# Kernel optimization log

Measured on AMD Instinct MI355X. Metric: run time of the kernel, lower is better.

The kernel has to match this reference:

```python
import jax, jax.numpy as jnp
import numpy as np

D_MODEL = 1024
NUM_HEADS = 16
D_K = D_MODEL // NUM_HEADS
NEG_INF = -1000000000.0


def setup_inputs() -> dict:
    key = jax.random.key(0)
    ks = jax.random.split(key, 12)
    B, S = 4, 2048
    scale = 1.0 / np.sqrt(D_MODEL)
    inp = {
        "query": jax.random.normal(ks[0], (B, S, D_MODEL), dtype=jnp.float32),
        "key": jax.random.normal(ks[1], (B, S, D_MODEL), dtype=jnp.float32),
        "value": jax.random.normal(ks[2], (B, S, D_MODEL), dtype=jnp.float32),
        # causal mask: True = keep (matches mask == False -> -1e9 fill)
        "mask": jnp.tril(jnp.ones((S, S), dtype=bool)),
        # torch nn.Linear: y = x @ W.T + b, W shape [out, in]
        "Wq": jax.random.normal(ks[3], (D_MODEL, D_MODEL), dtype=jnp.float32) * scale,
        "bq": jnp.zeros((D_MODEL,), dtype=jnp.float32),
        "Wk": jax.random.normal(ks[4], (D_MODEL, D_MODEL), dtype=jnp.float32) * scale,
        "bk": jnp.zeros((D_MODEL,), dtype=jnp.float32),
        "Wv": jax.random.normal(ks[5], (D_MODEL, D_MODEL), dtype=jnp.float32) * scale,
        "bv": jnp.zeros((D_MODEL,), dtype=jnp.float32),
        "Wo": jax.random.normal(ks[6], (D_MODEL, D_MODEL), dtype=jnp.float32) * scale,
        "bo": jnp.zeros((D_MODEL,), dtype=jnp.float32),
    }
    return inp


def _split_heads(x):
    # [B, S, D] -> [B, H, S, d_k]
    B, S, _ = x.shape
    return x.reshape(B, S, NUM_HEADS, D_K).transpose(0, 2, 1, 3)


def reference(query, key, value, mask, Wq, bq, Wk, bk, Wv, bv, Wo, bo):
    B, S, _ = query.shape
    q = _split_heads(query @ Wq.T + bq)
    k = _split_heads(key @ Wk.T + bk)
    v = _split_heads(value @ Wv.T + bv)
    # scores: [B, H, Sq, Sk]
    scores = jnp.einsum("bhqd,bhkd->bhqk", q, k) / jnp.sqrt(jnp.float32(D_K))
    scores = jnp.where(mask[None, None, :, :], scores, NEG_INF)
    p_attn = jax.nn.softmax(scores, axis=-1)
    x = jnp.einsum("bhqk,bhkd->bhqd", p_attn, v)
    x = x.transpose(0, 2, 1, 3).reshape(B, S, D_MODEL)
    return x @ Wo.T + bo
```

## Files before the change

### kernel.cpp

```cpp
#include <hip/hip_runtime.h>
#include <cstdint>
#include <cstddef>


typedef __attribute__((ext_vector_type(8))) short bf16x8;
typedef __attribute__((ext_vector_type(4))) float f32x4;
typedef __attribute__((ext_vector_type(16))) float f32x16;

__device__ __forceinline__ unsigned short f2bf(float f) {
  union { float f; unsigned u; } x; x.f = f;
  unsigned r = x.u + 0x7FFFu + ((x.u >> 16) & 1u);
  return (unsigned short)(r >> 16);
}

__device__ __forceinline__ unsigned cvtpk_bf16(float lo, float hi) {
  unsigned r;
  asm("v_cvt_pk_bf16_f32 %0, %1, %2" : "=v"(r) : "v"(lo), "v"(hi));
  return r;
}

__device__ __forceinline__ f32x16 mfma32(bf16x8 a, bf16x8 b, f32x16 c) {
  return __builtin_amdgcn_mfma_f32_32x32x16_bf16(a, b, c, 0, 0, 0);
}

__global__ __launch_bounds__(256)
void cast_w(const float* __restrict__ wq, const float* __restrict__ wk,
            const float* __restrict__ wv, const float* __restrict__ wo,
            unsigned short* __restrict__ wqb, unsigned short* __restrict__ wkb,
            unsigned short* __restrict__ wvb, unsigned short* __restrict__ wob) {
  constexpr int W4 = 1024 * 1024 / 4;
  const int i = blockIdx.x * 256 + threadIdx.x;
  const int r = i / W4;
  const int off = i - r * W4;
  const float* src = (r == 0) ? wq : (r == 1) ? wk : (r == 2) ? wv : wo;
  unsigned short* dst = (r == 0) ? wqb : (r == 1) ? wkb : (r == 2) ? wvb : wob;
  const float4 f = ((const float4*)src)[off];
  ushort4 o;
  o.x = f2bf(f.x); o.y = f2bf(f.y); o.z = f2bf(f.z); o.w = f2bf(f.w);
  ((ushort4*)dst)[off] = o;
}

__global__ __launch_bounds__(256)
void gemm_qkv(const float* __restrict__ Aq, const float* __restrict__ Ak,
              const float* __restrict__ Av,
              const unsigned short* __restrict__ Wq, const unsigned short* __restrict__ Wk,
              const unsigned short* __restrict__ Wv,
              const float* __restrict__ bq, const float* __restrict__ bk,
              const float* __restrict__ bv,
              unsigned short* __restrict__ Qp, unsigned short* __restrict__ Kp,
              unsigned short* __restrict__ Vt,
              int M, int N, int K) {
  constexpr int LDR = 72;
  __shared__ unsigned short As[128 * LDR];
  __shared__ unsigned short Bs[128 * LDR];
  const int which = blockIdx.x >> 9;
  const int bid = blockIdx.x & 511;
  const float* Af = (which == 0) ? Aq : (which == 1) ? Ak : Av;
  const unsigned short* Bw = (which == 0) ? Wq : (which == 1) ? Wk : Wv;
  const float* bias = (which == 0) ? bq : (which == 1) ? bk : bv;

  const int tid = threadIdx.x;
  const int lane = tid & 63;
  const int w = tid >> 6;
  const int wm = (w >> 1) * 64;
  const int wn = (w & 1) * 64;
  const int xcd = bid & 7, jj = bid >> 3;
  const int m0 = (xcd * 8 + (jj >> 3)) * 128;
  const int n0 = (jj & 7) * 128;
  const int l15 = lane & 15, l4 = lane >> 4;

  f32x4 acc[4][4] = {};

  for (int k0 = 0; k0 < K; k0 += 64) {
    float4 av[4][2];
    bf16x8 bst[4];
#pragma unroll
    for (int q = 0; q < 4; ++q) {
      const int c = q * 256 + tid;
      const int row = c >> 3, kc = (c & 7) * 8;
      const float4* ap = (const float4*)(Af + (size_t)(m0 + row) * K + k0 + kc);
      av[q][0] = ap[0];
      av[q][1] = ap[1];
      bst[q] = *(const bf16x8*)(Bw + (size_t)(n0 + row) * K + k0 + kc);
    }
    __syncthreads();
#pragma unroll
    for (int q = 0; q < 4; ++q) {
      const int c = q * 256 + tid;
      const int row = c >> 3, kc = (c & 7) * 8;
      union { bf16x8 v; unsigned u[4]; } p;
      p.u[0] = cvtpk_bf16(av[q][0].x, av[q][0].y);
      p.u[1] = cvtpk_bf16(av[q][0].z, av[q][0].w);
      p.u[2] = cvtpk_bf16(av[q][1].x, av[q][1].y);
      p.u[3] = cvtpk_bf16(av[q][1].z, av[q][1].w);
      *(bf16x8*)&As[row * LDR + kc] = p.v;
      *(bf16x8*)&Bs[row * LDR + kc] = bst[q];
    }
    __syncthreads();

#pragma unroll
    for (int kk = 0; kk < 2; ++kk) {
      bf16x8 af[4], bfr[4];
#pragma unroll
      for (int m = 0; m < 4; ++m)
        af[m] = *(const bf16x8*)&As[(wm + m * 16 + l15) * LDR + kk * 32 + l4 * 8];
#pragma unroll
      for (int n = 0; n < 4; ++n)
        bfr[n] = *(const bf16x8*)&Bs[(wn + n * 16 + l15) * LDR + kk * 32 + l4 * 8];
#pragma unroll
      for (int m = 0; m < 4; ++m)
#pragma unroll
        for (int n = 0; n < 4; ++n)
          acc[m][n] = __builtin_amdgcn_mfma_f32_16x16x32_bf16(af[m], bfr[n], acc[m][n], 0, 0, 0);
    }
  }

  const int crow = l4 * 4;
#pragma unroll
  for (int m = 0; m < 4; ++m) {
#pragma unroll
    for (int n = 0; n < 4; ++n) {
      const int col = n0 + wn + n * 16 + l15;
      const float bv_ = bias[col];
      if (which == 2) {
        constexpr int SS = 2048;
        const int rowb = m0 + wm + m * 16 + crow;
        const int b_ = rowb >> 11, s_ = rowb & (SS - 1);
        const int vrow = ((b_ << 4) + (col >> 6)) * 64 + (col & 63);
        uint2 pk;
        pk.x = cvtpk_bf16(acc[m][n][0] + bv_, acc[m][n][1] + bv_);
        pk.y = cvtpk_bf16(acc[m][n][2] + bv_, acc[m][n][3] + bv_);
        *(uint2*)&Vt[(size_t)vrow * SS + s_] = pk;
      } else {
        unsigned short* Cb = (which == 0) ? Qp : Kp;
        const float sc = (which == 0) ? 0.125f * 1.44269504f : 1.0f;
#pragma unroll
        for (int j = 0; j < 4; ++j) {
          const int row = m0 + wm + m * 16 + crow + j;
          Cb[(size_t)row * N + col] = f2bf((acc[m][n][j] + bv_) * sc);
        }
      }
    }
  }
}

__global__ __launch_bounds__(256)
void gemm_out(const unsigned short* __restrict__ Ab,
              const unsigned short* __restrict__ Bw,
              const float* __restrict__ bias,
              float* __restrict__ Cf,
              int M, int N, int K) {
  constexpr int LDR = 72;
  __shared__ unsigned short As[128 * LDR];
  __shared__ unsigned short Bs[128 * LDR];
  const int tid = threadIdx.x;
  const int lane = tid & 63;
  const int w = tid >> 6;
  const int wm = (w >> 1) * 64;
  const int wn = (w & 1) * 64;
  const int bid = blockIdx.x;
  const int xcd = bid & 7, jj = bid >> 3;
  const int m0 = (xcd * 8 + (jj >> 3)) * 128;
  const int n0 = (jj & 7) * 128;
  const int l15 = lane & 15, l4 = lane >> 4;

  f32x4 acc[4][4] = {};

  for (int k0 = 0; k0 < K; k0 += 64) {
    bf16x8 ast[4], bst[4];
#pragma unroll
    for (int q = 0; q < 4; ++q) {
      const int c = q * 256 + tid;
      const int row = c >> 3, kc = (c & 7) * 8;
      ast[q] = *(const bf16x8*)(Ab + (size_t)(m0 + row) * K + k0 + kc);
      bst[q] = *(const bf16x8*)(Bw + (size_t)(n0 + row) * K + k0 + kc);
    }
    __syncthreads();
#pragma unroll
    for (int q = 0; q < 4; ++q) {
      const int c = q * 256 + tid;
      const int row = c >> 3, kc = (c & 7) * 8;
      *(bf16x8*)&As[row * LDR + kc] = ast[q];
      *(bf16x8*)&Bs[row * LDR + kc] = bst[q];
    }
    __syncthreads();

#pragma unroll
    for (int kk = 0; kk < 2; ++kk) {
      bf16x8 af[4], bfr[4];
#pragma unroll
      for (int m = 0; m < 4; ++m)
        af[m] = *(const bf16x8*)&As[(wm + m * 16 + l15) * LDR + kk * 32 + l4 * 8];
#pragma unroll
      for (int n = 0; n < 4; ++n)
        bfr[n] = *(const bf16x8*)&Bs[(wn + n * 16 + l15) * LDR + kk * 32 + l4 * 8];
#pragma unroll
      for (int m = 0; m < 4; ++m)
#pragma unroll
        for (int n = 0; n < 4; ++n)
          acc[m][n] = __builtin_amdgcn_mfma_f32_16x16x32_bf16(af[m], bfr[n], acc[m][n], 0, 0, 0);
    }
  }

  const int crow = l4 * 4;
#pragma unroll
  for (int m = 0; m < 4; ++m) {
#pragma unroll
    for (int n = 0; n < 4; ++n) {
      const int col = n0 + wn + n * 16 + l15;
      const float bv_ = bias[col];
#pragma unroll
      for (int j = 0; j < 4; ++j) {
        const int row = m0 + wm + m * 16 + crow + j;
        Cf[(size_t)row * N + col] = acc[m][n][j] + bv_;
      }
    }
  }
}

__global__ __launch_bounds__(256)
void attn_fwd32b(const unsigned short* __restrict__ Qp,
                 const unsigned short* __restrict__ Kp,
                 const unsigned short* __restrict__ Vt,
                 unsigned short* __restrict__ Xo) {
  constexpr int S = 2048, Dm = 1024;
  const int bh = blockIdx.x & 63;
  const int g  = 15 - (int)(blockIdx.x >> 6);
  const int b = bh >> 4, h = bh & 15;
  const int w = threadIdx.x >> 6;
  const int lane = threadIdx.x & 63;
  const int l31 = lane & 31, hi = lane >> 5;
  const int qb = 4 * g + w;
  const int qrow = qb * 32 + l31;
  const int ntw = qb + 1;
  const int NT = 4 * g + 4;

  const unsigned short* qptr = Qp + (size_t)(b * S + qrow) * Dm + h * 64 + hi * 8;
  bf16x8 qf[4];
#pragma unroll
  for (int c = 0; c < 4; ++c) qf[c] = *(const bf16x8*)(qptr + c * 16);

  const unsigned short* kbase = Kp + (size_t)(b * S) * Dm + h * 64 + hi * 8;
  const unsigned short* vr0 = Vt + (size_t)(bh * 64 + l31) * S + hi * 8;
  const unsigned short* vr1 = vr0 + (size_t)32 * S;

  f32x16 ot0 = {}, ot1 = {};
  float m = -1e30f, l = 0.f;

  auto loadK = [&](bf16x8 (&kr)[4], int t) {
    const unsigned short* krow = kbase + (size_t)(t * 32 + l31) * Dm;
#pragma unroll
    for (int c = 0; c < 4; ++c) kr[c] = *(const bf16x8*)(krow + c * 16);
  };

  auto body = [&](bf16x8 (&kr)[4], int t) {
    const int kv0 = t * 32;
    const bf16x8 vf0a = *(const bf16x8*)(vr0 + kv0);
    const bf16x8 vf0b = *(const bf16x8*)(vr0 + kv0 + 16);
    const bf16x8 vf1a = *(const bf16x8*)(vr1 + kv0);
    const bf16x8 vf1b = *(const bf16x8*)(vr1 + kv0 + 16);
    f32x16 ts = {};
    __builtin_amdgcn_s_setprio(1);
#pragma unroll
    for (int c = 0; c < 4; ++c) ts = mfma32(kr[c], qf[c], ts);
    __builtin_amdgcn_s_setprio(0);
    if (t == ntw - 1) {
#pragma unroll
      for (int r = 0; r < 16; ++r) {
        const int kvp = kv0 + (r & 3) + 8 * (r >> 2) + 4 * hi;
        if (kvp > qrow) ts[r] = -1e9f;
      }
    }
    float pmax = ts[0];
#pragma unroll
    for (int r = 1; r < 16; ++r) pmax = fmaxf(pmax, ts[r]);
    pmax = fmaxf(pmax, __shfl_xor(pmax, 32));
    if (__any(pmax > m + 11.5f)) {
      const float mn = (pmax > m + 11.5f) ? pmax : m;
      const float fct = __builtin_amdgcn_exp2f(m - mn);
      m = mn; l *= fct;
#pragma unroll
      for (int r = 0; r < 16; ++r) { ot0[r] *= fct; ot1[r] *= fct; }
    }
    float p[16], ls = 0.f;
#pragma unroll
    for (int r = 0; r < 16; ++r) {
      p[r] = __builtin_amdgcn_exp2f(ts[r] - m);
      ls += p[r];
    }
    ls += __shfl_xor(ls, 32);
    l += ls;
    unsigned ua[8];
#pragma unroll
    for (int i = 0; i < 8; ++i) ua[i] = cvtpk_bf16(p[2 * i], p[2 * i + 1]);
    union FR { bf16x8 v; unsigned u[4]; } fr0, fr1;
    {
      unsigned sa = hi ? ua[0] : ua[2], sb = hi ? ua[1] : ua[3];
      unsigned xa = __shfl_xor(sa, 32), xb = __shfl_xor(sb, 32);
      fr0.u[0] = hi ? xa : ua[0]; fr0.u[1] = hi ? xb : ua[1];
      fr0.u[2] = hi ? ua[2] : xa; fr0.u[3] = hi ? ua[3] : xb;
      unsigned sc = hi ? ua[4] : ua[6], sd = hi ? ua[5] : ua[7];
      unsigned xc = __shfl_xor(sc, 32), xd = __shfl_xor(sd, 32);
      fr1.u[0] = hi ? xc : ua[4]; fr1.u[1] = hi ? xd : ua[5];
      fr1.u[2] = hi ? ua[6] : xc; fr1.u[3] = hi ? ua[7] : xd;
    }
    __builtin_amdgcn_s_setprio(1);
    ot0 = mfma32(vf0a, fr0.v, ot0);
    ot0 = mfma32(vf0b, fr1.v, ot0);
    ot1 = mfma32(vf1a, fr0.v, ot1);
    ot1 = mfma32(vf1b, fr1.v, ot1);
    __builtin_amdgcn_s_setprio(0);
  };

  bf16x8 kA[4], kB[4];
  loadK(kA, 0);
  for (int t = 0; t < NT; t += 2) {
    loadK(kB, t + 1);
    if (t < ntw) body(kA, t);
    __builtin_amdgcn_s_barrier();
    const int t2 = (t + 2 < NT) ? (t + 2) : (NT - 1);
    loadK(kA, t2);
    if (t + 1 < ntw) body(kB, t + 1);
    __builtin_amdgcn_s_barrier();
  }

  const float inv = 1.f / l;
  unsigned short* orow = Xo + (size_t)(b * S + qrow) * Dm + h * 64;
#pragma unroll
  for (int rq = 0; rq < 4; ++rq) {
    uint2 pr;
    pr.x = cvtpk_bf16(ot0[4 * rq + 0] * inv, ot0[4 * rq + 1] * inv);
    pr.y = cvtpk_bf16(ot0[4 * rq + 2] * inv, ot0[4 * rq + 3] * inv);
    *(uint2*)(orow + 8 * rq + 4 * hi) = pr;
    uint2 pr1;
    pr1.x = cvtpk_bf16(ot1[4 * rq + 0] * inv, ot1[4 * rq + 1] * inv);
    pr1.y = cvtpk_bf16(ot1[4 * rq + 2] * inv, ot1[4 * rq + 3] * inv);
    *(uint2*)(orow + 32 + 8 * rq + 4 * hi) = pr1;
  }
}

extern "C" void kernel_launch(void* const* d_in, const int* in_sizes, int n_in,
                              void* d_out, int out_size, void* d_ws, size_t ws_size,
                              hipStream_t stream) {
  const float* query = (const float*)d_in[0];
  const float* key   = (const float*)d_in[1];
  const float* value = (const float*)d_in[2];
  const float* Wq = (const float*)d_in[4];
  const float* bq = (const float*)d_in[5];
  const float* Wk = (const float*)d_in[6];
  const float* bk = (const float*)d_in[7];
  const float* Wv = (const float*)d_in[8];
  const float* bv = (const float*)d_in[9];
  const float* Wo = (const float*)d_in[10];
  const float* bo = (const float*)d_in[11];

  constexpr int B = 4, S = 2048, D = 1024;
  constexpr int M = B * S;
  const size_t MB = 1024u * 1024u;
  uint8_t* ws = (uint8_t*)d_ws;

  unsigned short* Wqb = (unsigned short*)(ws + 48 * MB);
  unsigned short* Wkb = (unsigned short*)(ws + 50 * MB);
  unsigned short* Wvb = (unsigned short*)(ws + 52 * MB);
  unsigned short* Wob = (unsigned short*)(ws + 54 * MB);
  unsigned short* Qp  = (unsigned short*)(ws + 56 * MB);
  unsigned short* Kp  = (unsigned short*)(ws + 72 * MB);
  unsigned short* Vt  = (unsigned short*)(ws + 32 * MB);
  unsigned short* Xat = (unsigned short*)(ws + 16 * MB);

  constexpr int W4 = D * D / 4;
  cast_w<<<4 * W4 / 256, 256, 0, stream>>>(Wq, Wk, Wv, Wo, Wqb, Wkb, Wvb, Wob);

  gemm_qkv<<<1536, 256, 0, stream>>>(query, key, value, Wqb, Wkb, Wvb,
                                     bq, bk, bv, Qp, Kp, Vt, M, D, D);

  attn_fwd32b<<<1024, 256, 0, stream>>>(Qp, Kp, Vt, Xat);

  gemm_out<<<512, 256, 0, stream>>>(Xat, Wob, bo, (float*)d_out, M, D, D);
}
```

Before: 245.5 us.

## Fuse QKV weight cast into GEMM load path and prefetch V alongside K

The separate bf16 cast of Wq/Wk/Wv is dropped. gemm_qkv now loads the fp32 weights directly and converts them in registers while staging to LDS, leaving only Wo cast in a smaller pre-kernel. This removes a kernel pass that wrote and reread about 6MB of bf16 weights, but the GEMM's weight reads double in size because fp32 is now loaded on every tile. Separately, the attention kernel double-buffers V fragments with K so V loads for the next tile are issued before the current body, at the cost of more registers.

```diff
diff --git a/kernel.cpp b/kernel.cpp
--- a/kernel.cpp
+++ b/kernel.cpp
@@ -24,27 +24,19 @@
 }
 
 __global__ __launch_bounds__(256)
-void cast_w(const float* __restrict__ wq, const float* __restrict__ wk,
-            const float* __restrict__ wv, const float* __restrict__ wo,
-            unsigned short* __restrict__ wqb, unsigned short* __restrict__ wkb,
-            unsigned short* __restrict__ wvb, unsigned short* __restrict__ wob) {
-  constexpr int W4 = 1024 * 1024 / 4;
+void cast_wo(const float* __restrict__ wo, unsigned short* __restrict__ wob) {
   const int i = blockIdx.x * 256 + threadIdx.x;
-  const int r = i / W4;
-  const int off = i - r * W4;
-  const float* src = (r == 0) ? wq : (r == 1) ? wk : (r == 2) ? wv : wo;
-  unsigned short* dst = (r == 0) ? wqb : (r == 1) ? wkb : (r == 2) ? wvb : wob;
-  const float4 f = ((const float4*)src)[off];
+  const float4 f = ((const float4*)wo)[i];
   ushort4 o;
   o.x = f2bf(f.x); o.y = f2bf(f.y); o.z = f2bf(f.z); o.w = f2bf(f.w);
-  ((ushort4*)dst)[off] = o;
+  ((ushort4*)wob)[i] = o;
 }
 
 __global__ __launch_bounds__(256)
 void gemm_qkv(const float* __restrict__ Aq, const float* __restrict__ Ak,
               const float* __restrict__ Av,
-              const unsigned short* __restrict__ Wq, const unsigned short* __restrict__ Wk,
-              const unsigned short* __restrict__ Wv,
+              const float* __restrict__ Wq, const float* __restrict__ Wk,
+              const float* __restrict__ Wv,
               const float* __restrict__ bq, const float* __restrict__ bk,
               const float* __restrict__ bv,
               unsigned short* __restrict__ Qp, unsigned short* __restrict__ Kp,
@@ -56,7 +48,7 @@
   const int which = blockIdx.x >> 9;
   const int bid = blockIdx.x & 511;
   const float* Af = (which == 0) ? Aq : (which == 1) ? Ak : Av;
-  const unsigned short* Bw = (which == 0) ? Wq : (which == 1) ? Wk : Wv;
+  const float* Bf = (which == 0) ? Wq : (which == 1) ? Wk : Wv;
   const float* bias = (which == 0) ? bq : (which == 1) ? bk : bv;
 
   const int tid = threadIdx.x;
@@ -72,8 +64,7 @@
   f32x4 acc[4][4] = {};
 
   for (int k0 = 0; k0 < K; k0 += 64) {
-    float4 av[4][2];
-    bf16x8 bst[4];
+    float4 av[4][2], bv4[4][2];
 #pragma unroll
     for (int q = 0; q < 4; ++q) {
       const int c = q * 256 + tid;
@@ -81,20 +72,26 @@
       const float4* ap = (const float4*)(Af + (size_t)(m0 + row) * K + k0 + kc);
       av[q][0] = ap[0];
       av[q][1] = ap[1];
-      bst[q] = *(const bf16x8*)(Bw + (size_t)(n0 + row) * K + k0 + kc);
+      const float4* bp = (const float4*)(Bf + (size_t)(n0 + row) * K + k0 + kc);
+      bv4[q][0] = bp[0];
+      bv4[q][1] = bp[1];
     }
     __syncthreads();
 #pragma unroll
     for (int q = 0; q < 4; ++q) {
       const int c = q * 256 + tid;
       const int row = c >> 3, kc = (c & 7) * 8;
-      union { bf16x8 v; unsigned u[4]; } p;
+      union { bf16x8 v; unsigned u[4]; } p, pb;
       p.u[0] = cvtpk_bf16(av[q][0].x, av[q][0].y);
       p.u[1] = cvtpk_bf16(av[q][0].z, av[q][0].w);
       p.u[2] = cvtpk_bf16(av[q][1].x, av[q][1].y);
       p.u[3] = cvtpk_bf16(av[q][1].z, av[q][1].w);
+      pb.u[0] = cvtpk_bf16(bv4[q][0].x, bv4[q][0].y);
+      pb.u[1] = cvtpk_bf16(bv4[q][0].z, bv4[q][0].w);
+      pb.u[2] = cvtpk_bf16(bv4[q][1].x, bv4[q][1].y);
+      pb.u[3] = cvtpk_bf16(bv4[q][1].z, bv4[q][1].w);
       *(bf16x8*)&As[row * LDR + kc] = p.v;
-      *(bf16x8*)&Bs[row * LDR + kc] = bst[q];
+      *(bf16x8*)&Bs[row * LDR + kc] = pb.v;
     }
     __syncthreads();
 
@@ -252,13 +249,16 @@
 #pragma unroll
     for (int c = 0; c < 4; ++c) kr[c] = *(const bf16x8*)(krow + c * 16);
   };
-
-  auto body = [&](bf16x8 (&kr)[4], int t) {
+  auto loadV = [&](bf16x8 (&vr)[4], int t) {
     const int kv0 = t * 32;
-    const bf16x8 vf0a = *(const bf16x8*)(vr0 + kv0);
-    const bf16x8 vf0b = *(const bf16x8*)(vr0 + kv0 + 16);
-    const bf16x8 vf1a = *(const bf16x8*)(vr1 + kv0);
-    const bf16x8 vf1b = *(const bf16x8*)(vr1 + kv0 + 16);
+    vr[0] = *(const bf16x8*)(vr0 + kv0);
+    vr[1] = *(const bf16x8*)(vr0 + kv0 + 16);
+    vr[2] = *(const bf16x8*)(vr1 + kv0);
+    vr[3] = *(const bf16x8*)(vr1 + kv0 + 16);
+  };
+
+  auto body = [&](bf16x8 (&kr)[4], bf16x8 (&vr)[4], int t) {
+    const int kv0 = t * 32;
     f32x16 ts = {};
     __builtin_amdgcn_s_setprio(1);
 #pragma unroll
@@ -305,22 +305,22 @@
       fr1.u[2] = hi ? ua[6] : xc; fr1.u[3] = hi ? ua[7] : xd;
     }
     __builtin_amdgcn_s_setprio(1);
-    ot0 = mfma32(vf0a, fr0.v, ot0);
-    ot0 = mfma32(vf0b, fr1.v, ot0);
-    ot1 = mfma32(vf1a, fr0.v, ot1);
-    ot1 = mfma32(vf1b, fr1.v, ot1);
+    ot0 = mfma32(vr[0], fr0.v, ot0);
+    ot0 = mfma32(vr[1], fr1.v, ot0);
+    ot1 = mfma32(vr[2], fr0.v, ot1);
+    ot1 = mfma32(vr[3], fr1.v, ot1);
     __builtin_amdgcn_s_setprio(0);
   };
 
-  bf16x8 kA[4], kB[4];
-  loadK(kA, 0);
+  bf16x8 kA[4], kB[4], vA[4], vB[4];
+  loadK(kA, 0); loadV(vA, 0);
   for (int t = 0; t < NT; t += 2) {
-    loadK(kB, t + 1);
-    if (t < ntw) body(kA, t);
+    loadK(kB, t + 1); loadV(vB, t + 1);
+    if (t < ntw) body(kA, vA, t);
     __builtin_amdgcn_s_barrier();
     const int t2 = (t + 2 < NT) ? (t + 2) : (NT - 1);
-    loadK(kA, t2);
-    if (t + 1 < ntw) body(kB, t + 1);
+    loadK(kA, t2); loadV(vA, t2);
+    if (t + 1 < ntw) body(kB, vB, t + 1);
     __builtin_amdgcn_s_barrier();
   }
 
@@ -359,9 +359,6 @@
   const size_t MB = 1024u * 1024u;
   uint8_t* ws = (uint8_t*)d_ws;
 
-  unsigned short* Wqb = (unsigned short*)(ws + 48 * MB);
-  unsigned short* Wkb = (unsigned short*)(ws + 50 * MB);
-  unsigned short* Wvb = (unsigned short*)(ws + 52 * MB);
   unsigned short* Wob = (unsigned short*)(ws + 54 * MB);
   unsigned short* Qp  = (unsigned short*)(ws + 56 * MB);
   unsigned short* Kp  = (unsigned short*)(ws + 72 * MB);
@@ -369,9 +366,9 @@
   unsigned short* Xat = (unsigned short*)(ws + 16 * MB);
 
   constexpr int W4 = D * D / 4;
-  cast_w<<<4 * W4 / 256, 256, 0, stream>>>(Wq, Wk, Wv, Wo, Wqb, Wkb, Wvb, Wob);
-
-  gemm_qkv<<<1536, 256, 0, stream>>>(query, key, value, Wqb, Wkb, Wvb,
+  cast_wo<<<W4 / 256, 256, 0, stream>>>(Wo, Wob);
+
+  gemm_qkv<<<1536, 256, 0, stream>>>(query, key, value, Wq, Wk, Wv,
                                      bq, bk, bv, Qp, Kp, Vt, M, D, D);
 
   attn_fwd32b<<<1024, 256, 0, stream>>>(Qp, Kp, Vt, Xat);
```

Measured after the change: 265.6 us. 1.08x slower.
